# Optimization experiments

Measured on AMD Instinct MI355X. Metric: run time of the kernel, lower is better.

The kernel has to match this reference:

```python
import jax, jax.numpy as jnp
import numpy as np


def setup_inputs() -> dict:
    key = jax.random.key(0)
    kD, kx, kc = jax.random.split(key, 3)
    B, N, I, O = 8, 20000, 64, 64
    KM = 8 * 32  # k_bands * m_samples = 256
    D = jax.random.normal(kD, (B, N, KM), dtype=jnp.float32)
    x = jax.random.normal(kx, (B, N, I), dtype=jnp.float32)
    coefficients = jax.random.normal(kc, (1, O, I, KM), dtype=jnp.float32)
    return {"D": D, "x": x, "coefficients": coefficients}


def reference(D, x, coefficients):
    # D: (B, N, M), x: (B, N, I), coefficients: (1, O, I, M)
    # Original: C = diag_embed(coeff) -> (1,O,I,M,M); einsum('boimj,bomi->boij')
    # Since C is diagonal in (m, j), that einsum is an elementwise scale:
    #   C_Dt_x[b,o,i,m] = coeff[o,i,m] * Dt_x[b,m,i]
    # and the final contraction + channel-sum is:
    #   out[b,n,o] = (1/sqrt(M)) * sum_m D[b,n,m] * sum_i coeff[o,i,m] * Dt_x[b,m,i]
    M = D.shape[2]
    coeff = coefficients[0]                              # (O, I, M)
    Dt_x = jnp.einsum('bnm,bni->bmi', D, x)              # (B, M, I)
    S = jnp.einsum('oim,bmi->bom', coeff, Dt_x)          # (B, O, M)
    out = jnp.einsum('bnm,bom->bno', D, S) / jnp.sqrt(jnp.asarray(M, D.dtype))
    return out  # (B, N, O)
```

## Files before the change

kernel.cpp:

```cpp
#include <hip/hip_runtime.h>

#define B 8
#define N 20000
#define M 256
#define I 64
#define O 64
#define MI (M * I)
#define KT 32
#define SSS 264
#define MSW(m) ((m) ^ (((m) >> 3) & 7))

typedef __attribute__((ext_vector_type(8))) short   bf16x8;
typedef __attribute__((ext_vector_type(4))) float   f32x4;
typedef __attribute__((ext_vector_type(4))) unsigned int uint4v;

__device__ __forceinline__ unsigned pk2bf(float lo, float hi) {
    unsigned r;
    asm("v_cvt_pk_bf16_f32 %0, %1, %2" : "=v"(r) : "v"(lo), "v"(hi));
    return r;
}

__device__ __forceinline__ unsigned short f2bf(float v) {
    unsigned a = __float_as_uint(v);
    return (unsigned short)((a + 0x7fffu + ((a >> 16) & 1u)) >> 16);
}

__global__ __launch_bounds__(256) void stage1(const float* __restrict__ Dg,
                                              const float* __restrict__ xg,
                                              float* __restrict__ partial,
                                              int chunk) {
    const int b = blockIdx.y, s = blockIdx.x;
    const int n0 = s * chunk;
    const int nend = min(n0 + chunk, N);
    const int tid = threadIdx.x;
    const int lane = tid & 63;
    const int w = tid >> 6;
    const bool interior = (n0 + chunk) <= N;

    __shared__ unsigned short sD[2][4 * 256 * 8];
    __shared__ unsigned short sX[2][4 * 64 * 8];

    f32x4 acc[4][4];
#pragma unroll
    for (int a = 0; a < 4; ++a)
#pragma unroll
        for (int v = 0; v < 4; ++v) acc[a][v] = (f32x4){0.f, 0.f, 0.f, 0.f};

    const float* Db = Dg + (size_t)b * N * M;
    const float* xb = xg + (size_t)b * N * I;

    const int steps = (nend > n0) ? (nend - n0 + KT - 1) / KT : 0;

    float4 dreg[8];
    float  xreg[8];

    auto load_fast = [&](int nbase) {
        const float* dp = &Db[(size_t)(nbase + w * 8) * M + lane * 4];
        const float* xp = &xb[(size_t)(nbase + w * 8) * I + lane];
#pragma unroll
        for (int q = 0; q < 8; ++q) {
            dreg[q] = *(const float4*)(dp + (size_t)q * M);
            xreg[q] = xp[(size_t)q * I];
        }
    };
    auto load_clamped = [&](int nbase) {
#pragma unroll
        for (int q = 0; q < 8; ++q) {
            const int nc = min(nbase + w * 8 + q, N - 1);
            dreg[q] = *(const float4*)&Db[(size_t)nc * M + lane * 4];
            xreg[q] = xb[(size_t)nc * I + lane];
        }
    };

    if (steps > 0) {
        if (interior) load_fast(n0); else load_clamped(n0);

        for (int t = 0; t < steps; ++t) {
            const int nb = n0 + t * KT;
            const int cur = t & 1;
            if (!interior) {
#pragma unroll
                for (int q = 0; q < 8; ++q)
                    if (nb + w * 8 + q >= nend) {
                        dreg[q] = make_float4(0.f, 0.f, 0.f, 0.f);
                        xreg[q] = 0.f;
                    }
            }
#pragma unroll
            for (int j = 0; j < 4; ++j) {
                uint4v cell;
#pragma unroll
                for (int e = 0; e < 4; ++e)
                    cell[e] = pk2bf(((const float*)&dreg[2 * e])[j],
                                    ((const float*)&dreg[2 * e + 1])[j]);
                const int m = lane * 4 + j;
                *(uint4v*)&sD[cur][((size_t)w * 256 + MSW(m)) * 8] = cell;
            }
            {
                uint4v cell;
#pragma unroll
                for (int e = 0; e < 4; ++e)
                    cell[e] = pk2bf(xreg[2 * e], xreg[2 * e + 1]);
                *(uint4v*)&sX[cur][((size_t)w * 64 + lane) * 8] = cell;
            }
            if (t + 1 < steps) {
                if (interior) load_fast(nb + KT); else load_clamped(nb + KT);
            }
            __syncthreads();
            const int g = lane >> 4;
            bf16x8 bfr[4];
#pragma unroll
            for (int v = 0; v < 4; ++v)
                bfr[v] = *(const bf16x8*)&sX[cur][((size_t)g * 64 + v * 16 + (lane & 15)) * 8];
#pragma unroll
            for (int sm = 0; sm < 4; ++sm) {
                const int mm = w * 64 + sm * 16 + (lane & 15);
                bf16x8 afr = *(const bf16x8*)&sD[cur][((size_t)g * 256 + MSW(mm)) * 8];
#pragma unroll
                for (int v = 0; v < 4; ++v)
                    acc[sm][v] = __builtin_amdgcn_mfma_f32_16x16x32_bf16(
                        afr, bfr[v], acc[sm][v], 0, 0, 0);
            }
        }
    }

    float* p = partial + ((size_t)s * B + b) * MI;
#pragma unroll
    for (int sm = 0; sm < 4; ++sm)
#pragma unroll
        for (int v = 0; v < 4; ++v)
#pragma unroll
            for (int r = 0; r < 4; ++r) {
                const int m = w * 64 + sm * 16 + ((lane >> 4) << 2) + r;
                const int i = v * 16 + (lane & 15);
                p[m * I + i] = acc[sm][v][r];
            }
}

__global__ __launch_bounds__(256) void reduce_partials(const float* __restrict__ partial,
                                                       float* __restrict__ dtx,
                                                       int nsplit) {
    const int bb = blockIdx.y;
    const int j = blockIdx.x * 256 + threadIdx.x;
    const float* p = partial + (size_t)bb * MI + j;
    float sum = 0.f;
#pragma unroll 4
    for (int s = 0; s < nsplit; ++s)
        sum += p[(size_t)s * B * MI];
    dtx[(size_t)bb * MI + j] = sum;
}

__global__ __launch_bounds__(256) void stage2(const float* __restrict__ coeff,
                                              const float* __restrict__ dtx,
                                              unsigned short* __restrict__ ST) {
    const int g = blockIdx.x * 256 + threadIdx.x;
    const int b = g >> 14;
    const int rem = g & 16383;
    const int o = rem >> 8;
    const int m = rem & 255;
    const float* dt = dtx + (size_t)b * MI + (size_t)m * I;
    const float* cf = coeff + (size_t)o * I * M + m;
    float acc = 0.f;
#pragma unroll 8
    for (int i = 0; i < I; ++i)
        acc = fmaf(cf[(size_t)i * M], dt[i], acc);
    ST[((size_t)b * O + o) * M + m] = f2bf(acc * 0.0625f);
}

__global__ __launch_bounds__(256) void stage3(const float* __restrict__ Dg,
                                              const unsigned short* __restrict__ STg,
                                              float* __restrict__ outg) {
    const int b = blockIdx.y;
    const int n0 = blockIdx.x * 256;
    const int tid = threadIdx.x;
    const int lane = tid & 63;
    const int w = tid >> 6;

    __shared__ unsigned short sS[64 * SSS];

    {
        const int o = tid >> 2, seg = (tid & 3) * 64;
        const unsigned short* src = STg + ((size_t)b * O + o) * M + seg;
        unsigned short* dst = &sS[o * SSS + seg];
#pragma unroll
        for (int c = 0; c < 8; ++c)
            *(uint4v*)&dst[c * 8] = *(const uint4v*)&src[c * 8];
    }

    f32x4 acc[4][4];
#pragma unroll
    for (int a = 0; a < 4; ++a)
#pragma unroll
        for (int v = 0; v < 4; ++v) acc[a][v] = (f32x4){0.f, 0.f, 0.f, 0.f};

    __syncthreads();

    const float* Db = Dg + (size_t)b * N * M;
    const int k8 = (lane >> 4) << 3;

#pragma unroll 1
    for (int ks = 0; ks < 8; ++ks) {
        const int kb = ks * 32 + k8;
        bf16x8 bfr[4];
#pragma unroll
        for (int v = 0; v < 4; ++v)
            bfr[v] = *(const bf16x8*)&sS[(v * 16 + (lane & 15)) * SSS + kb];
#pragma unroll
        for (int sn = 0; sn < 4; ++sn) {
            int n = n0 + w * 64 + sn * 16 + (lane & 15);
            n = min(n, N - 1);
            const float* ap = Db + (size_t)n * M + kb;
            const float4 f0 = *(const float4*)ap;
            const float4 f1 = *(const float4*)(ap + 4);
            uint4v pk = {pk2bf(f0.x, f0.y), pk2bf(f0.z, f0.w),
                         pk2bf(f1.x, f1.y), pk2bf(f1.z, f1.w)};
            bf16x8 afr = __builtin_bit_cast(bf16x8, pk);
#pragma unroll
            for (int v = 0; v < 4; ++v)
                acc[sn][v] = __builtin_amdgcn_mfma_f32_16x16x32_bf16(
                    afr, bfr[v], acc[sn][v], 0, 0, 0);
        }
    }

#pragma unroll
    for (int sn = 0; sn < 4; ++sn)
#pragma unroll
        for (int v = 0; v < 4; ++v)
#pragma unroll
            for (int r = 0; r < 4; ++r) {
                const int n = n0 + w * 64 + sn * 16 + ((lane >> 4) << 2) + r;
                if (n < N)
                    outg[((size_t)b * N + n) * O + v * 16 + (lane & 15)] = acc[sn][v][r];
            }
}

extern "C" void kernel_launch(void* const* d_in, const int* in_sizes, int n_in,
                              void* d_out, int out_size, void* d_ws, size_t ws_size,
                              hipStream_t stream) {
    const float* Dg    = (const float*)d_in[0];
    const float* xg    = (const float*)d_in[1];
    const float* coeff = (const float*)d_in[2];
    float* outg = (float*)d_out;

    float* base = (float*)d_ws;
    float* dtx = base;
    unsigned short* ST = (unsigned short*)(base + B * MI);
    float* partial = base + B * MI + B * MI / 2;

    const size_t fixed = (size_t)B * MI * 4 + (size_t)B * MI * 2;
    const size_t per   = (size_t)B * MI * sizeof(float);
    int split = 1;
    if (ws_size > fixed) {
        size_t cap = (ws_size - fixed) / per;
        split = (int)(cap < 1 ? 1 : (cap > 96 ? 96 : cap));
    }
    int chunk = ((N + split - 1) / split + KT - 1) & ~(KT - 1);

    stage1<<<dim3(split, B), 256, 0, stream>>>(Dg, xg, partial, chunk);
    reduce_partials<<<dim3(MI / 256, B), 256, 0, stream>>>(partial, dtx, split);
    stage2<<<dim3((B * O * M) / 256), 256, 0, stream>>>(coeff, dtx, ST);
    stage3<<<dim3((N + 255) / 256, B), 256, 0, stream>>>(Dg, ST, outg);
}
```

Measured before the change: 106.1 us.

## Make each wave own its LDS slice to drop block barriers in stage1

```diff
diff --git a/kernel.cpp b/kernel.cpp
--- a/kernel.cpp
+++ b/kernel.cpp
@@ -35,10 +35,12 @@
     const int tid = threadIdx.x;
     const int lane = tid & 63;
     const int w = tid >> 6;
+    const int lg = lane >> 4;
+    const int l15 = lane & 15;
     const bool interior = (n0 + chunk) <= N;
 
-    __shared__ unsigned short sD[2][4 * 256 * 8];
-    __shared__ unsigned short sX[2][4 * 64 * 8];
+    __shared__ unsigned short sD[4][4 * 64 * 8];
+    __shared__ unsigned short sX[4][4 * 64 * 8];
 
     f32x4 acc[4][4];
 #pragma unroll
@@ -46,76 +48,72 @@
 #pragma unroll
         for (int v = 0; v < 4; ++v) acc[a][v] = (f32x4){0.f, 0.f, 0.f, 0.f};
 
-    const float* Db = Dg + (size_t)b * N * M;
+    const float* Db = Dg + (size_t)b * N * M + w * 64;
     const float* xb = xg + (size_t)b * N * I;
 
     const int steps = (nend > n0) ? (nend - n0 + KT - 1) / KT : 0;
 
     float4 dreg[8];
-    float  xreg[8];
+    float4 xreg[8];
 
     auto load_fast = [&](int nbase) {
-        const float* dp = &Db[(size_t)(nbase + w * 8) * M + lane * 4];
-        const float* xp = &xb[(size_t)(nbase + w * 8) * I + lane];
+        const float* dp = &Db[(size_t)(nbase + 8 * lg) * M + 4 * l15];
+        const float* xp = &xb[(size_t)(nbase + 8 * lg) * I + 4 * l15];
 #pragma unroll
         for (int q = 0; q < 8; ++q) {
             dreg[q] = *(const float4*)(dp + (size_t)q * M);
-            xreg[q] = xp[(size_t)q * I];
+            xreg[q] = *(const float4*)(xp + (size_t)q * I);
         }
     };
     auto load_clamped = [&](int nbase) {
 #pragma unroll
         for (int q = 0; q < 8; ++q) {
-            const int nc = min(nbase + w * 8 + q, N - 1);
-            dreg[q] = *(const float4*)&Db[(size_t)nc * M + lane * 4];
-            xreg[q] = xb[(size_t)nc * I + lane];
+            const int nc = min(nbase + 8 * lg + q, N - 1);
+            dreg[q] = *(const float4*)&Db[(size_t)nc * M + 4 * l15];
+            xreg[q] = *(const float4*)&xb[(size_t)nc * I + 4 * l15];
         }
     };
+
+    unsigned short* wD = sD[w];
+    unsigned short* wX = sX[w];
 
     if (steps > 0) {
         if (interior) load_fast(n0); else load_clamped(n0);
 
         for (int t = 0; t < steps; ++t) {
             const int nb = n0 + t * KT;
-            const int cur = t & 1;
             if (!interior) {
 #pragma unroll
                 for (int q = 0; q < 8; ++q)
-                    if (nb + w * 8 + q >= nend) {
+                    if (nb + 8 * lg + q >= nend) {
                         dreg[q] = make_float4(0.f, 0.f, 0.f, 0.f);
-                        xreg[q] = 0.f;
+                        xreg[q] = make_float4(0.f, 0.f, 0.f, 0.f);
                     }
             }
 #pragma unroll
             for (int j = 0; j < 4; ++j) {
-                uint4v cell;
-#pragma unroll
-                for (int e = 0; e < 4; ++e)
-                    cell[e] = pk2bf(((const float*)&dreg[2 * e])[j],
-                                    ((const float*)&dreg[2 * e + 1])[j]);
-                const int m = lane * 4 + j;
-                *(uint4v*)&sD[cur][((size_t)w * 256 + MSW(m)) * 8] = cell;
-            }
-            {
-                uint4v cell;
-#pragma unroll
-                for (int e = 0; e < 4; ++e)
-                    cell[e] = pk2bf(xreg[2 * e], xreg[2 * e + 1]);
-                *(uint4v*)&sX[cur][((size_t)w * 64 + lane) * 8] = cell;
+                uint4v cd, cx;
+#pragma unroll
+                for (int e = 0; e < 4; ++e) {
+                    cd[e] = pk2bf(((const float*)&dreg[2 * e])[j],
+                                  ((const float*)&dreg[2 * e + 1])[j]);
+                    cx[e] = pk2bf(((const float*)&xreg[2 * e])[j],
+                                  ((const float*)&xreg[2 * e + 1])[j]);
+                }
+                const int c = MSW(4 * l15 + j);
+                *(uint4v*)&wD[((size_t)lg * 64 + c) * 8] = cd;
+                *(uint4v*)&wX[((size_t)lg * 64 + c) * 8] = cx;
             }
             if (t + 1 < steps) {
                 if (interior) load_fast(nb + KT); else load_clamped(nb + KT);
             }
-            __syncthreads();
-            const int g = lane >> 4;
             bf16x8 bfr[4];
 #pragma unroll
             for (int v = 0; v < 4; ++v)
-                bfr[v] = *(const bf16x8*)&sX[cur][((size_t)g * 64 + v * 16 + (lane & 15)) * 8];
+                bfr[v] = *(const bf16x8*)&wX[((size_t)lg * 64 + MSW(v * 16 + l15)) * 8];
 #pragma unroll
             for (int sm = 0; sm < 4; ++sm) {
-                const int mm = w * 64 + sm * 16 + (lane & 15);
-                bf16x8 afr = *(const bf16x8*)&sD[cur][((size_t)g * 256 + MSW(mm)) * 8];
+                bf16x8 afr = *(const bf16x8*)&wD[((size_t)lg * 64 + MSW(sm * 16 + l15)) * 8];
 #pragma unroll
                 for (int v = 0; v < 4; ++v)
                     acc[sm][v] = __builtin_amdgcn_mfma_f32_16x16x32_bf16(
@@ -249,12 +247,13 @@
 
     const size_t fixed = (size_t)B * MI * 4 + (size_t)B * MI * 2;
     const size_t per   = (size_t)B * MI * sizeof(float);
-    int split = 1;
+    int cap = 1;
     if (ws_size > fixed) {
-        size_t cap = (ws_size - fixed) / per;
-        split = (int)(cap < 1 ? 1 : (cap > 96 ? 96 : cap));
-    }
-    int chunk = ((N + split - 1) / split + KT - 1) & ~(KT - 1);
+        size_t c = (ws_size - fixed) / per;
+        cap = (int)(c < 1 ? 1 : (c > 128 ? 128 : c));
+    }
+    int chunk = (((N + cap - 1) / cap) + KT - 1) & ~(KT - 1);
+    int split = (N + chunk - 1) / chunk;
 
     stage1<<<dim3(split, B), 256, 0, stream>>>(Dg, xg, partial, chunk);
     reduce_partials<<<dim3(MI / 256, B), 256, 0, stream>>>(partial, dtx, split);
```

Measured after the change: 116.3 us. +9.7%, slower.
